# Kernel optimization log

Hardware: AMD Instinct MI355X
Metric: run time of the kernel (lower is better)

Reference implementation:

```python
import jax, jax.numpy as jnp
import numpy as np
import math

DIM = 32
CODEBOOK_SIZE = 16384
LOG_N = int(math.log(CODEBOOK_SIZE, 2))  # 14
LOGVAR_MIN, LOGVAR_MAX = -30.0, 20.0
TOL = 0.5
BETA = 1.0
LAM = 1.0
LAM_MIN = 1.0
LAM_MAX = 1.0
HALF_LOG_2PI = 0.5 * math.log(2.0 * math.pi)


def setup_inputs() -> dict:
    key = jax.random.key(0)
    k1, k2, k3 = jax.random.split(key, 3)
    z = jax.random.normal(k1, (4, 512, 512), dtype=jnp.float32)
    noise = jax.random.normal(k2, (2048, 256), dtype=jnp.float32)
    # prior_samples buffer: standard-normal codebook [K, DIM]
    codebook = jax.random.normal(k3, (CODEBOOK_SIZE, DIM), dtype=jnp.float32)
    return {"z": z, "noise": noise, "codebook": codebook}


def _forward(z, noise, codebook):
    z_shape = z.shape
    zf = z.reshape(-1, z_shape[-1])                       # [N_tok, 2*DIM*cb]
    cb_num = zf.shape[-1] // (2 * DIM)                    # codebook_num
    mu, logvar = jnp.split(zf, 2, axis=-1)                # each [N_tok, DIM*cb]
    logvar = jnp.clip(logvar, LOGVAR_MIN, LOGVAR_MAX)
    std = jnp.exp(0.5 * logvar)
    var = jnp.exp(logvar)

    # ---- quant_gaussian ----
    zhat_g = mu + noise * std                             # reparam sample
    kl2 = 1.4426 * 0.5 * (mu * mu + var - 1.0 - logvar)
    kl2 = kl2.reshape(-1, DIM, cb_num).sum(axis=1)        # [N_tok, cb]
    ge = (kl2 > LOG_N + TOL).astype(kl2.dtype) * LAM_MAX
    eq = ((kl2 <= LOG_N + TOL) & (kl2 >= LOG_N - TOL)).astype(kl2.dtype)
    le = (kl2 < LOG_N - TOL).astype(kl2.dtype) * LAM_MIN
    kl_loss = jnp.mean(ge * kl2 + eq * kl2 + le * kl2) * LAM

    # ---- quant_vq (Gaussian log-likelihood-ratio codebook search) ----
    # rows: (token, codebook_num) pairs, each with a DIM-dim Gaussian
    mu_r = mu.reshape(-1, DIM, cb_num).transpose(0, 2, 1).reshape(-1, DIM)    # [N, DIM]
    std_r = std.reshape(-1, DIM, cb_num).transpose(0, 2, 1).reshape(-1, DIM)  # [N, DIM]
    inv_var = 1.0 / (std_r * std_r)                                           # [N, DIM]

    c = codebook                                          # [K, DIM]
    c2 = c * c
    # sum_d Normal(mu, std).log_prob(c) expanded into GEMMs over DIM:
    #   -sum log std - DIM/2*log(2pi) - 0.5*(c^2 - 2 c mu + mu^2) / var
    termA = -jnp.sum(jnp.log(std_r), axis=-1) - DIM * HALF_LOG_2PI            # [N]
    quad = 0.5 * (jnp.einsum('nd,kd->nk', inv_var, c2)
                  - 2.0 * jnp.einsum('nd,kd->nk', mu_r * inv_var, c)
                  + jnp.sum(mu_r * mu_r * inv_var, axis=-1, keepdims=True))   # [N, K]
    prior_lp = jnp.sum(-0.5 * c2 - HALF_LOG_2PI, axis=-1)                     # [K]
    perturbed = termA[:, None] - quad - BETA * prior_lp[None, :]              # [N, K]

    indices = jnp.argmax(perturbed, axis=1)               # [N]
    zhat_v = c[indices]                                   # [N, DIM]

    zhat_v = zhat_v.reshape(-1, cb_num, DIM).transpose(0, 2, 1).reshape(-1, cb_num * DIM)
    zhat_v = zhat_v.reshape(*z_shape[:-1], -1)            # [..., DIM*cb]
    zhat_g = zhat_g.reshape(*z_shape[:-1], -1)
    indices = indices.reshape(*z_shape[:-1], cb_num)

    # straight-through estimator (use_ste=True); vq branch is no_grad in torch
    zhat = zhat_g - jax.lax.stop_gradient(zhat_g) + jax.lax.stop_gradient(zhat_v)
    return zhat, kl_loss, indices


def reference(z, noise, codebook):
    return _forward(z, noise, codebook)
```

## Files before the change

kernel.cpp:

```cpp
#include <hip/hip_runtime.h>
#include <math.h>


typedef _Float16 half8 __attribute__((ext_vector_type(8)));
typedef float f32x4 __attribute__((ext_vector_type(4)));

#define DIM 32
#define NROWS 16384
#define KSIZE 16384
#define NSPLIT 16
#define SPLITK 1024
#define NCOL 256

#define WS_M1   0
#define WS_KL   256
#define WS_CN1  512
#define WS_CN2  1536
#define WS_PQ   4096
#define WS_AH   (WS_PQ + 4194304)
#define WS_BH   (WS_AH + 2097152)
#define WS_W1   (WS_BH + 2097152)

__global__ __launch_bounds__(256) void prep_kernel(const float* __restrict__ cb,
                                                   const float* __restrict__ z,
                                                   _Float16* __restrict__ Bh,
                                                   float* __restrict__ M1,
                                                   float* __restrict__ CN1,
                                                   float* __restrict__ CN2,
                                                   float* __restrict__ PQ,
                                                   _Float16* __restrict__ Ah,
                                                   double* __restrict__ klsum) {
  const int w = threadIdx.x >> 6, l = threadIdx.x & 63;
  const int sub = l >> 5, d = l & 31;
  if (blockIdx.x < 512) {
    __shared__ float lm[8][DIM];
    float m = 0.0f;
#pragma unroll
    for (int i = 0; i < 4; ++i) {
      const int k = blockIdx.x * 32 + i * 8 + w * 2 + sub;
      const float c = cb[k * DIM + d];
      const int key = k & 7;
      const int sc = (d >> 3) ^ key;
      const int sq = (4 + (d >> 3)) ^ key;
      Bh[(size_t)k * 64 + sc * 8 + (d & 7)] = (_Float16)c;
      Bh[(size_t)k * 64 + sq * 8 + (d & 7)] = (_Float16)(c * c);
      m = fmaxf(m, fabsf(c));
      float s2 = c * c, s4 = c * c * c * c;
#pragma unroll
      for (int mask = 1; mask <= 16; mask <<= 1) {
        s2 += __shfl_xor(s2, mask);
        s4 += __shfl_xor(s4, mask);
      }
      if (d == 0) {
        const int col = (k >> 10) * 16 + (k & 15);
        atomicMax((unsigned*)&CN1[col], __float_as_uint(sqrtf(s2)));
        atomicMax((unsigned*)&CN2[col], __float_as_uint(sqrtf(s4)));
      }
    }
    lm[threadIdx.x >> 5][d] = m;
    __syncthreads();
    if (threadIdx.x < DIM) {
      float x = lm[0][threadIdx.x];
#pragma unroll
      for (int i = 1; i < 8; ++i) x = fmaxf(x, lm[i][threadIdx.x]);
      atomicMax((unsigned*)&M1[threadIdx.x], __float_as_uint(x));
    }
  } else {
    const int blk = blockIdx.x - 512;
    double kacc = 0.0;
#pragma unroll 1
    for (int i = 0; i < 4; ++i) {
      const int row = blk * 32 + i * 8 + w * 2 + sub;
      const int t = row >> 3, c = row & 7;
      const float mu = z[t * 512 + d * 8 + c];
      float lv = z[t * 512 + 256 + d * 8 + c];
      lv = fminf(fmaxf(lv, -30.0f), 20.0f);
      const float stdv = expf(0.5f * lv);
      const float iv = 1.0f / (stdv * stdv);
      const float p = mu * iv;
      const float q = 0.5f * (1.0f - iv);
      PQ[(size_t)row * 64 + d] = p;
      PQ[(size_t)row * 64 + 32 + d] = q;
      Ah[(size_t)row * 64 + d] = (_Float16)p;
      Ah[(size_t)row * 64 + 32 + d] = (_Float16)q;
      kacc += (double)(mu * mu + stdv * stdv - 1.0f - lv);
    }
#pragma unroll
    for (int off = 32; off > 0; off >>= 1) kacc += __shfl_down(kacc, off);
    __shared__ double wsum[4];
    if (l == 0) wsum[w] = kacc;
    __syncthreads();
    if (threadIdx.x == 0)
      atomicAdd(klsum, (wsum[0] + wsum[1]) + (wsum[2] + wsum[3]));
  }
}

__device__ __forceinline__ void gload_lds16(const _Float16* g, _Float16* l) {
  __builtin_amdgcn_global_load_lds(
      (__attribute__((address_space(1))) void*)(g),
      (__attribute__((address_space(3))) void*)(l), 16, 0, 0);
}

__global__ __launch_bounds__(256, 2) void filter_kernel(const _Float16* __restrict__ Ah,
                                                        const _Float16* __restrict__ Bh,
                                                        _Float16* __restrict__ W1) {
  __shared__ _Float16 sB[2][16384];
  const int tid = threadIdx.x;
  const int lane = tid & 63;
  const int wave = tid >> 6;
  const int split = blockIdx.y;
  const int rowbase = blockIdx.x * 512 + wave * 128;
  const int c16 = lane & 15, quad = lane >> 4;

  const _Float16* gB = Bh + (size_t)split * SPLITK * 64;

#pragma unroll
  for (int j = 0; j < 8; ++j)
    gload_lds16(gB + j * 2048 + tid * 8, &sB[0][j * 2048 + tid * 8]);

  half8 uh0[8], uh1[8];
#pragma unroll
  for (int rt = 0; rt < 8; ++rt) {
    const size_t abase = (size_t)(rowbase + rt * 16 + c16) * 64 + quad * 8;
    uh0[rt] = *(const half8*)(Ah + abase);
    uh1[rt] = *(const half8*)(Ah + abase + 32);
  }

  float a1[8][4];
#pragma unroll
  for (int rt = 0; rt < 8; ++rt)
#pragma unroll
    for (int r = 0; r < 4; ++r) a1[rt][r] = -INFINITY;

  const f32x4 fzero = {0.f, 0.f, 0.f, 0.f};
  const int key = c16 & 7;
  const int rs0h = c16 * 64 + (quad ^ key) * 8;
  const int rs1h = c16 * 64 + ((quad + 4) ^ key) * 8;

  __syncthreads();

#pragma unroll 1
  for (int ch = 0; ch < 4; ++ch) {
    if (ch < 3) {
      const _Float16* src = gB + (size_t)(ch + 1) * 16384;
      _Float16* dst = &sB[(ch + 1) & 1][0];
#pragma unroll
      for (int j = 0; j < 8; ++j)
        gload_lds16(src + j * 2048 + tid * 8, dst + j * 2048 + tid * 8);
    }
    const _Float16* buf = &sB[ch & 1][0];
#pragma unroll 1
    for (int tp = 0; tp < 8; ++tp) {
      const _Float16* b0 = buf + (2 * tp) * 1024;
      const _Float16* b1 = b0 + 1024;
      const half8 x0 = *(const half8*)(b0 + rs0h);
      const half8 x1 = *(const half8*)(b0 + rs1h);
      const half8 y0 = *(const half8*)(b1 + rs0h);
      const half8 y1 = *(const half8*)(b1 + rs1h);
#pragma unroll
      for (int rt = 0; rt < 8; ++rt) {
        f32x4 h0 = __builtin_amdgcn_mfma_f32_16x16x32_f16(uh0[rt], x0, fzero, 0, 0, 0);
        h0 = __builtin_amdgcn_mfma_f32_16x16x32_f16(uh1[rt], x1, h0, 0, 0, 0);
        f32x4 h1 = __builtin_amdgcn_mfma_f32_16x16x32_f16(uh0[rt], y0, fzero, 0, 0, 0);
        h1 = __builtin_amdgcn_mfma_f32_16x16x32_f16(uh1[rt], y1, h1, 0, 0, 0);
#pragma unroll
        for (int r = 0; r < 4; ++r)
          a1[rt][r] = fmaxf(fmaxf(h0[r], h1[r]), a1[rt][r]);
      }
    }
    __syncthreads();
  }

#pragma unroll
  for (int rt = 0; rt < 8; ++rt)
#pragma unroll
    for (int r = 0; r < 4; ++r) {
      const int row_r = rowbase + rt * 16 + quad * 4 + r;
      W1[((size_t)split * NROWS + row_r) * 16 + c16] =
          (_Float16)fmaxf(a1[rt][r], -65504.0f);
    }
}

__device__ __forceinline__ float exact_score(const float4* __restrict__ cb4,
                                             const float4* __restrict__ spq,
                                             int k) {
  float s0 = 0.0f, s1 = 0.0f, s2 = 0.0f, s3 = 0.0f;
#pragma unroll
  for (int m = 0; m < 8; ++m) {
    const float4 cv = cb4[k * 8 + m];
    const float4 pv = spq[m];
    const float4 qv = spq[8 + m];
    s0 = fmaf(cv.x, fmaf(qv.x, cv.x, pv.x), s0);
    s1 = fmaf(cv.y, fmaf(qv.y, cv.y, pv.y), s1);
    s2 = fmaf(cv.z, fmaf(qv.z, cv.z, pv.z), s2);
    s3 = fmaf(cv.w, fmaf(qv.w, cv.w, pv.w), s3);
  }
  return (s0 + s1) + (s2 + s3);
}

__global__ __launch_bounds__(256, 4) void merge_kernel(const float* __restrict__ PQ,
                                                       const float* __restrict__ cb,
                                                       const _Float16* __restrict__ W1,
                                                       const float* __restrict__ CN1,
                                                       const float* __restrict__ CN2,
                                                       const double* __restrict__ klsum,
                                                       float* __restrict__ out0,
                                                       float* __restrict__ out1,
                                                       float* __restrict__ out2) {
  __shared__ float4 spq_s[4][16];
  const int lane = threadIdx.x & 63;
  const int wave = threadIdx.x >> 6;
  const int row = blockIdx.x * 4 + wave;

  if (lane < 16)
    spq_s[wave][lane] = ((const float4*)(PQ + (size_t)row * 64))[lane];
  __syncthreads();
  const float4* spq = spq_s[wave];
  const float4* __restrict__ cb4 = (const float4*)cb;

  float sp = 0.0f, sq = 0.0f;
  if (lane < DIM) {
    const float pd = ((const float*)spq)[lane];
    const float qd = ((const float*)spq)[32 + lane];
    sp = pd * pd;
    sq = qd * qd;
  }
#pragma unroll
  for (int off = 1; off < 32; off <<= 1) {
    sp += __shfl_xor(sp, off);
    sq += __shfl_xor(sq, off);
  }
  const float pn = sqrtf(__shfl(sp, 0));
  const float qn = sqrtf(__shfl(sq, 0));

  float w[4];
#pragma unroll
  for (int i = 0; i < 4; ++i)
    w[i] = (float)W1[((size_t)(i * 4 + (lane >> 4)) * NROWS + row) * 16 + (lane & 15)];
  float As = fmaxf(fmaxf(w[0], w[1]), fmaxf(w[2], w[3]));
#pragma unroll
  for (int off = 1; off < 64; off <<= 1) As = fmaxf(As, __shfl_xor(As, off));
  const float slack = 2e-5f * (fabsf(As) + 1.0f) + 1e-3f;

  float bt[4];
#pragma unroll
  for (int i = 0; i < 4; ++i) {
    const int col = i * 64 + lane;
    bt[i] = 1.05e-3f * (pn * CN1[col] + qn * CN2[col]) + slack
            + 5e-4f * fabsf(w[i]);
  }

  int done_col = -1;
#pragma unroll
  for (int i = 0; i < 4; ++i) {
    if (done_col < 0) {
      const unsigned long long m = __ballot(w[i] == As);
      if (m) done_col = i * 64 + __builtin_ctzll(m);
    }
  }
  const int k0 = (done_col >> 4) * SPLITK + lane * 16 + (done_col & 15);
  float best = exact_score(cb4, spq, k0);
  int bk = k0;
#pragma unroll
  for (int off = 1; off < 64; off <<= 1) {
    const float ov = __shfl_xor(best, off);
    const int ok = __shfl_xor(bk, off);
    if (ov > best || (ov == best && ok < bk)) { best = ov; bk = ok; }
  }
  const float Estar = best;

#pragma unroll 1
  for (int i = 0; i < 4; ++i) {
    unsigned long long m = __ballot(w[i] + bt[i] >= Estar);
    if ((done_col >> 6) == i) m &= ~(1ull << (done_col & 63));
    while (m) {
      const int e = __builtin_ctzll(m);
      m &= m - 1;
      const int col = i * 64 + e;
      const int k = (col >> 4) * SPLITK + lane * 16 + (col & 15);
      const float sc = exact_score(cb4, spq, k);
      if (sc > best || (sc == best && k < bk)) { best = sc; bk = k; }
    }
  }
#pragma unroll
  for (int off = 1; off < 64; off <<= 1) {
    const float ov = __shfl_xor(best, off);
    const int ok = __shfl_xor(bk, off);
    if (ov > best || (ov == best && ok < bk)) { best = ov; bk = ok; }
  }
  if (lane == 0) out2[row] = (float)bk;
  const int tt = row >> 3, cc = row & 7;
  if (lane < DIM) out0[tt * 256 + lane * 8 + cc] = cb[bk * DIM + lane];
  if (blockIdx.x == 0 && threadIdx.x == 0)
    out1[0] = (float)(klsum[0] * (1.4426 * 0.5) / (double)NROWS);
}

extern "C" void kernel_launch(void* const* d_in, const int* in_sizes, int n_in,
                              void* d_out, int out_size, void* d_ws, size_t ws_size,
                              hipStream_t stream) {
  const float* z  = (const float*)d_in[0];
  const float* cb = (const float*)d_in[2];

  char* ws = (char*)d_ws;
  float*      M1 = (float*)(ws + WS_M1);
  double* klsum  = (double*)(ws + WS_KL);
  float*     CN1 = (float*)(ws + WS_CN1);
  float*     CN2 = (float*)(ws + WS_CN2);
  float*      PQ = (float*)(ws + WS_PQ);
  _Float16*   Ah = (_Float16*)(ws + WS_AH);
  _Float16*   Bh = (_Float16*)(ws + WS_BH);
  _Float16*   W1 = (_Float16*)(ws + WS_W1);

  float* out0 = (float*)d_out;
  float* out1 = out0 + 524288;
  float* out2 = out1 + 1;

  (void)hipMemsetAsync(ws, 0, 4096, stream);
  prep_kernel<<<1024, 256, 0, stream>>>(cb, z, Bh, M1, CN1, CN2, PQ, Ah, klsum);
  dim3 fgrid(32, NSPLIT);
  filter_kernel<<<fgrid, 256, 0, stream>>>(Ah, Bh, W1);
  merge_kernel<<<NROWS / 4, 256, 0, stream>>>(PQ, cb, W1, CN1, CN2, klsum,
                                              out0, out1, out2);
}
```

Baseline: 133.7 us.

## Halve codebook split size to tighten filter bounds and drop LDS double-buffering

Splits the codebook into 32 slices of 512 entries instead of 16 slices of 1024, so each row keeps 512 fp16 max-bins instead of 256. Finer bins are meant to let the merge kernel's bound test prune more columns, so fewer candidates need exact rescoring. Each filter block now loads its whole 64KB slice into LDS in one go and drops the double-buffered chunk pipeline. The grid has twice as many blocks. In exchange the W1 buffer doubles, the merge kernel reads twice as much per row, and load latency is no longer overlapped with MFMA work.

```diff
diff --git a/kernel.cpp b/kernel.cpp
--- a/kernel.cpp
+++ b/kernel.cpp
@@ -8,15 +8,15 @@
 #define DIM 32
 #define NROWS 16384
 #define KSIZE 16384
-#define NSPLIT 16
-#define SPLITK 1024
-#define NCOL 256
+#define NHS 32
+#define HSK 512
+#define NCOL 512
 
 #define WS_M1   0
 #define WS_KL   256
-#define WS_CN1  512
-#define WS_CN2  1536
-#define WS_PQ   4096
+#define WS_CN1  1024
+#define WS_CN2  3072
+#define WS_PQ   8192
 #define WS_AH   (WS_PQ + 4194304)
 #define WS_BH   (WS_AH + 2097152)
 #define WS_W1   (WS_BH + 2097152)
@@ -52,7 +52,7 @@
         s4 += __shfl_xor(s4, mask);
       }
       if (d == 0) {
-        const int col = (k >> 10) * 16 + (k & 15);
+        const int col = (k >> 9) * 16 + (k & 15);
         atomicMax((unsigned*)&CN1[col], __float_as_uint(sqrtf(s2)));
         atomicMax((unsigned*)&CN2[col], __float_as_uint(sqrtf(s4)));
       }
@@ -104,19 +104,18 @@
 __global__ __launch_bounds__(256, 2) void filter_kernel(const _Float16* __restrict__ Ah,
                                                         const _Float16* __restrict__ Bh,
                                                         _Float16* __restrict__ W1) {
-  __shared__ _Float16 sB[2][16384];
+  __shared__ _Float16 sB[32768];
   const int tid = threadIdx.x;
   const int lane = tid & 63;
   const int wave = tid >> 6;
-  const int split = blockIdx.y;
+  const int hs = blockIdx.y;
   const int rowbase = blockIdx.x * 512 + wave * 128;
   const int c16 = lane & 15, quad = lane >> 4;
 
-  const _Float16* gB = Bh + (size_t)split * SPLITK * 64;
-
-#pragma unroll
-  for (int j = 0; j < 8; ++j)
-    gload_lds16(gB + j * 2048 + tid * 8, &sB[0][j * 2048 + tid * 8]);
+  const _Float16* gB = Bh + (size_t)hs * HSK * 64;
+#pragma unroll
+  for (int j = 0; j < 16; ++j)
+    gload_lds16(gB + j * 2048 + tid * 8, &sB[j * 2048 + tid * 8]);
 
   half8 uh0[8], uh1[8];
 #pragma unroll
@@ -140,35 +139,23 @@
   __syncthreads();
 
 #pragma unroll 1
-  for (int ch = 0; ch < 4; ++ch) {
-    if (ch < 3) {
-      const _Float16* src = gB + (size_t)(ch + 1) * 16384;
-      _Float16* dst = &sB[(ch + 1) & 1][0];
-#pragma unroll
-      for (int j = 0; j < 8; ++j)
-        gload_lds16(src + j * 2048 + tid * 8, dst + j * 2048 + tid * 8);
-    }
-    const _Float16* buf = &sB[ch & 1][0];
-#pragma unroll 1
-    for (int tp = 0; tp < 8; ++tp) {
-      const _Float16* b0 = buf + (2 * tp) * 1024;
-      const _Float16* b1 = b0 + 1024;
-      const half8 x0 = *(const half8*)(b0 + rs0h);
-      const half8 x1 = *(const half8*)(b0 + rs1h);
-      const half8 y0 = *(const half8*)(b1 + rs0h);
-      const half8 y1 = *(const half8*)(b1 + rs1h);
-#pragma unroll
-      for (int rt = 0; rt < 8; ++rt) {
-        f32x4 h0 = __builtin_amdgcn_mfma_f32_16x16x32_f16(uh0[rt], x0, fzero, 0, 0, 0);
-        h0 = __builtin_amdgcn_mfma_f32_16x16x32_f16(uh1[rt], x1, h0, 0, 0, 0);
-        f32x4 h1 = __builtin_amdgcn_mfma_f32_16x16x32_f16(uh0[rt], y0, fzero, 0, 0, 0);
-        h1 = __builtin_amdgcn_mfma_f32_16x16x32_f16(uh1[rt], y1, h1, 0, 0, 0);
-#pragma unroll
-        for (int r = 0; r < 4; ++r)
-          a1[rt][r] = fmaxf(fmaxf(h0[r], h1[r]), a1[rt][r]);
-      }
-    }
-    __syncthreads();
+  for (int tp = 0; tp < 16; ++tp) {
+    const _Float16* b0 = sB + (2 * tp) * 1024;
+    const _Float16* b1 = b0 + 1024;
+    const half8 x0 = *(const half8*)(b0 + rs0h);
+    const half8 x1 = *(const half8*)(b0 + rs1h);
+    const half8 y0 = *(const half8*)(b1 + rs0h);
+    const half8 y1 = *(const half8*)(b1 + rs1h);
+#pragma unroll
+    for (int rt = 0; rt < 8; ++rt) {
+      f32x4 h0 = __builtin_amdgcn_mfma_f32_16x16x32_f16(uh0[rt], x0, fzero, 0, 0, 0);
+      h0 = __builtin_amdgcn_mfma_f32_16x16x32_f16(uh1[rt], x1, h0, 0, 0, 0);
+      f32x4 h1 = __builtin_amdgcn_mfma_f32_16x16x32_f16(uh0[rt], y0, fzero, 0, 0, 0);
+      h1 = __builtin_amdgcn_mfma_f32_16x16x32_f16(uh1[rt], y1, h1, 0, 0, 0);
+#pragma unroll
+      for (int r = 0; r < 4; ++r)
+        a1[rt][r] = fmaxf(fmaxf(h0[r], h1[r]), a1[rt][r]);
+    }
   }
 
 #pragma unroll
@@ -176,7 +163,7 @@
 #pragma unroll
     for (int r = 0; r < 4; ++r) {
       const int row_r = rowbase + rt * 16 + quad * 4 + r;
-      W1[((size_t)split * NROWS + row_r) * 16 + c16] =
+      W1[((size_t)hs * NROWS + row_r) * 16 + c16] =
           (_Float16)fmaxf(a1[rt][r], -65504.0f);
     }
 }
@@ -233,18 +220,20 @@
   const float pn = sqrtf(__shfl(sp, 0));
   const float qn = sqrtf(__shfl(sq, 0));
 
-  float w[4];
-#pragma unroll
-  for (int i = 0; i < 4; ++i)
+  float w[8];
+#pragma unroll
+  for (int i = 0; i < 8; ++i)
     w[i] = (float)W1[((size_t)(i * 4 + (lane >> 4)) * NROWS + row) * 16 + (lane & 15)];
-  float As = fmaxf(fmaxf(w[0], w[1]), fmaxf(w[2], w[3]));
+  float As = w[0];
+#pragma unroll
+  for (int i = 1; i < 8; ++i) As = fmaxf(As, w[i]);
 #pragma unroll
   for (int off = 1; off < 64; off <<= 1) As = fmaxf(As, __shfl_xor(As, off));
   const float slack = 2e-5f * (fabsf(As) + 1.0f) + 1e-3f;
 
-  float bt[4];
-#pragma unroll
-  for (int i = 0; i < 4; ++i) {
+  float bt[8];
+#pragma unroll
+  for (int i = 0; i < 8; ++i) {
     const int col = i * 64 + lane;
     bt[i] = 1.05e-3f * (pn * CN1[col] + qn * CN2[col]) + slack
             + 5e-4f * fabsf(w[i]);
@@ -252,13 +241,13 @@
 
   int done_col = -1;
 #pragma unroll
-  for (int i = 0; i < 4; ++i) {
+  for (int i = 0; i < 8; ++i) {
     if (done_col < 0) {
       const unsigned long long m = __ballot(w[i] == As);
       if (m) done_col = i * 64 + __builtin_ctzll(m);
     }
   }
-  const int k0 = (done_col >> 4) * SPLITK + lane * 16 + (done_col & 15);
+  const int k0 = (done_col >> 4) * HSK + (lane & 31) * 16 + (done_col & 15);
   float best = exact_score(cb4, spq, k0);
   int bk = k0;
 #pragma unroll
@@ -270,14 +259,14 @@
   const float Estar = best;
 
 #pragma unroll 1
-  for (int i = 0; i < 4; ++i) {
+  for (int i = 0; i < 8; ++i) {
     unsigned long long m = __ballot(w[i] + bt[i] >= Estar);
     if ((done_col >> 6) == i) m &= ~(1ull << (done_col & 63));
     while (m) {
       const int e = __builtin_ctzll(m);
       m &= m - 1;
       const int col = i * 64 + e;
-      const int k = (col >> 4) * SPLITK + lane * 16 + (col & 15);
+      const int k = (col >> 4) * HSK + (lane & 31) * 16 + (col & 15);
       const float sc = exact_score(cb4, spq, k);
       if (sc > best || (sc == best && k < bk)) { best = sc; bk = k; }
     }
@@ -315,9 +304,9 @@
   float* out1 = out0 + 524288;
   float* out2 = out1 + 1;
 
-  (void)hipMemsetAsync(ws, 0, 4096, stream);
+  (void)hipMemsetAsync(ws, 0, 8192, stream);
   prep_kernel<<<1024, 256, 0, stream>>>(cb, z, Bh, M1, CN1, CN2, PQ, Ah, klsum);
-  dim3 fgrid(32, NSPLIT);
+  dim3 fgrid(32, NHS);
   filter_kernel<<<fgrid, 256, 0, stream>>>(Ah, Bh, W1);
   merge_kernel<<<NROWS / 4, 256, 0, stream>>>(PQ, cb, W1, CN1, CN2, klsum,
                                               out0, out1, out2);
```

Measured after the change: 133.9 us. Within noise of the previous version (+0.2%).
